# Kernel tuning notes

Measured on AMD Instinct MI355X. Metric: run time of the kernel, lower is better.

## Reference

```python
import jax, jax.numpy as jnp
import numpy as np

B, C, A, N = 4, 128, 64, 4096


def setup_inputs() -> dict:
    key = jax.random.key(0)
    ks = jax.random.split(key, 7)
    x = jax.random.normal(ks[0], (B, C, N), dtype=jnp.float32)
    # Conv1d kernel_size=1 == pointwise linear; store weights as [out, in]
    s = 1.0 / np.sqrt(C)
    Wq = jax.random.uniform(ks[1], (A, C), jnp.float32, -s, s)
    bq = jax.random.uniform(ks[2], (A,), jnp.float32, -s, s)
    Wk = jax.random.uniform(ks[3], (A, C), jnp.float32, -s, s)
    bk = jax.random.uniform(ks[4], (A,), jnp.float32, -s, s)
    Wv = jax.random.uniform(ks[5], (C, C), jnp.float32, -s, s)
    bv = jax.random.uniform(ks[6], (C,), jnp.float32, -s, s)
    return {"x": x, "Wq": Wq, "bq": bq, "Wk": Wk, "bk": bk, "Wv": Wv, "bv": bv}


def reference(x, Wq, bq, Wk, bk, Wv, bv):
    # 1x1 conv projections: [B,C,N] -> [B,A,N] / [B,C,N]
    q = jnp.einsum('ac,bcn->ban', Wq, x) + bq[None, :, None]
    k = jnp.einsum('ac,bcn->ban', Wk, x) + bk[None, :, None]
    v = jnp.einsum('oc,bcn->bon', Wv, x) + bv[None, :, None]
    # scores: q^T k -> [B, N, N], softmax over last dim (keys)
    attn = jax.nn.softmax(jnp.einsum('ban,bam->bnm', q, k), axis=-1)
    # out = attn @ v^T -> [B, N, C], transpose back to [B, C, N]
    ctx = jnp.einsum('bnm,bcm->bcn', attn, v)
    return x + ctx
```

## Files before the change

kernel.cpp:

```cpp
#include <hip/hip_runtime.h>
#include <stdint.h>

#define BB 4
#define CC 128
#define AA 64
#define NN 4096
#define LOG2E 1.44269504088896f

using half8  = __attribute__((ext_vector_type(8))) _Float16;
using f32x4  = __attribute__((ext_vector_type(4))) float;
using f32x16 = __attribute__((ext_vector_type(16))) float;
using u32x4  = __attribute__((ext_vector_type(4))) uint32_t;

__device__ __forceinline__ float fexp2(float x) {
  float r; asm("v_exp_f32 %0, %1" : "=v"(r) : "v"(x)); return r;
}


__global__ __launch_bounds__(256) void proj_kernel(
    const float* __restrict__ x,
    const float* __restrict__ Wq, const float* __restrict__ bq,
    const float* __restrict__ Wk, const float* __restrict__ bk,
    const float* __restrict__ Wv, const float* __restrict__ bv,
    _Float16* __restrict__ qfrag, _Float16* __restrict__ kfrag,
    _Float16* __restrict__ vfrag)
{
  __shared__ _Float16 xT[64][136];
  __shared__ _Float16 bounce[4][64][72];
  const int tid = threadIdx.x;
  const int wid = tid >> 6, lane = tid & 63;
  const int g = lane >> 4, lr = lane & 15;
  const int c32 = lane & 31, h = lane >> 5;
  const int b = blockIdx.x & 3, nt = blockIdx.x >> 2;
  const int n0 = nt * 64;

  for (int i = 0; i < 8; ++i) {
    int idx = i * 256 + tid;
    int c = idx >> 4, s = idx & 15;
    float4 xv = *(const float4*)(x + (size_t)(b * CC + c) * NN + n0 + s * 4);
    xT[s*4+0][c] = (_Float16)xv.x;
    xT[s*4+1][c] = (_Float16)xv.y;
    xT[s*4+2][c] = (_Float16)xv.z;
    xT[s*4+3][c] = (_Float16)xv.w;
  }
  __syncthreads();

  const float* Wp; const float* bp; int rbase;
  if (wid == 0)      { Wp = Wq; bp = bq; rbase = 0; }
  else if (wid == 1) { Wp = Wk; bp = bk; rbase = 0; }
  else               { Wp = Wv; bp = bv; rbase = (wid - 2) * 64; }
  const float oscale = (wid == 0) ? LOG2E : 1.0f;

  const f32x4 zero4 = {0.f, 0.f, 0.f, 0.f};
  f32x4 acc[4][4];
  #pragma unroll
  for (int i = 0; i < 4; ++i)
    #pragma unroll
    for (int j = 0; j < 4; ++j) acc[i][j] = zero4;

  #pragma unroll
  for (int ks = 0; ks < 4; ++ks) {
    half8 af[4];
    #pragma unroll
    for (int nf = 0; nf < 4; ++nf)
      af[nf] = *(const half8*)&xT[nf*16 + lr][ks*32 + g*8];
    half8 bfr[4];
    #pragma unroll
    for (int rf = 0; rf < 4; ++rf) {
      const float* wrow = Wp + (size_t)(rbase + rf*16 + lr) * CC + ks*32 + g*8;
      float4 w0 = *(const float4*)wrow;
      float4 w1 = *(const float4*)(wrow + 4);
      half8 t;
      t[0]=(_Float16)w0.x; t[1]=(_Float16)w0.y; t[2]=(_Float16)w0.z; t[3]=(_Float16)w0.w;
      t[4]=(_Float16)w1.x; t[5]=(_Float16)w1.y; t[6]=(_Float16)w1.z; t[7]=(_Float16)w1.w;
      bfr[rf] = t;
    }
    #pragma unroll
    for (int nf = 0; nf < 4; ++nf)
      #pragma unroll
      for (int rf = 0; rf < 4; ++rf)
        acc[nf][rf] = __builtin_amdgcn_mfma_f32_16x16x32_f16(af[nf], bfr[rf], acc[nf][rf], 0, 0, 0);
  }

  #pragma unroll
  for (int rf = 0; rf < 4; ++rf) {
    float bias = bp[rbase + rf*16 + lr];
    #pragma unroll
    for (int nf = 0; nf < 4; ++nf)
      #pragma unroll
      for (int r = 0; r < 4; ++r) {
        float val = (acc[nf][rf][r] + bias) * oscale;
        if (wid < 2) bounce[wid][nf*16 + 4*g + r][rf*16 + lr] = (_Float16)val;
        else         bounce[wid][rf*16 + lr][nf*16 + 4*g + r] = (_Float16)val;
      }
  }
  __syncthreads();

  if (wid == 0) {
    _Float16* dst = qfrag + (size_t)(b*128 + 2*nt) * 2048;
    #pragma unroll
    for (int t = 0; t < 8; ++t) {
      int n32t = t >> 2, ks = t & 3;
      half8 v8 = *(const half8*)&bounce[0][n32t*32 + c32][ks*16 + h*8];
      *(half8*)(dst + (size_t)(n32t*4 + ks)*512 + lane*8) = v8;
    }
  } else if (wid == 1) {
    _Float16* dst = kfrag + (size_t)(b*64 + nt) * 4096;
    #pragma unroll
    for (int t = 0; t < 8; ++t) {
      int mt = t >> 2, ks = t & 3;
      half8 v8 = *(const half8*)&bounce[1][mt*32 + c32][ks*16 + h*8];
      *(half8*)(dst + (size_t)(mt*4 + ks)*512 + lane*8) = v8;
    }
  } else {
    _Float16* dst = vfrag + (size_t)(b*64 + nt) * 8192;
    #pragma unroll
    for (int t = 0; t < 8; ++t) {
      int ms = t >> 1, ctl = t & 1;
      int ct = (wid - 2)*2 + ctl;
      half8 v8 = *(const half8*)&bounce[wid][ctl*32 + c32][ms*16 + h*8];
      *(half8*)(dst + (size_t)(ms*4 + ct)*512 + lane*8) = v8;
    }
  }
}

__global__ __launch_bounds__(512, 2) void attn_kernel(
    const float* __restrict__ x,
    const _Float16* __restrict__ qfrag, const _Float16* __restrict__ kfrag,
    const _Float16* __restrict__ vfrag, float* __restrict__ out)
{
  __shared__ __align__(16) float smem_f[24576 + 384 + 8448];
  float* ctxb  = smem_f;
  float* statb = smem_f + 24576;
  float* ctxw  = smem_f + 24960;

  const int tid = threadIdx.x;
  const int wid = tid >> 6, lane = tid & 63;
  const int c32 = lane & 31;
  const int h = lane >> 5;
  const bool hb = (h != 0);
  const int sub = wid >> 2;
  const int qr  = wid & 3;
  const int b = blockIdx.x & 3, qt = blockIdx.x >> 2;
  const int n0 = qt * 64;

  half8 qf[4];
  const _Float16* qfb = qfrag + (size_t)(b*128 + qt*2 + sub) * 2048;
  #pragma unroll
  for (int ks = 0; ks < 4; ++ks)
    qf[ks] = *(const half8*)(qfb + ks*512 + lane*8);

  const _Float16* kfb = kfrag + (size_t)(b*64 + qr*16) * 4096;
  const _Float16* vfb = vfrag + (size_t)(b*64 + qr*16) * 8192;

  f32x16 ctx[4];
  #pragma unroll
  for (int ct = 0; ct < 4; ++ct)
    #pragma unroll
    for (int r = 0; r < 16; ++r) ctx[ct][r] = 0.f;
  float run_m = -1e30f, run_l = 0.f;

  half8 kf[2][4];
  #pragma unroll
  for (int mt = 0; mt < 2; ++mt)
    #pragma unroll
    for (int ks = 0; ks < 4; ++ks)
      kf[mt][ks] = *(const half8*)(kfb + (size_t)(mt*4 + ks)*512 + lane*8);

  for (int it = 0; it < 16; ++it) {
    const _Float16* vt = vfb + (size_t)it * 8192;
    half8 vfA[2][4];
    #pragma unroll
    for (int ms = 0; ms < 2; ++ms)
      #pragma unroll
      for (int ct = 0; ct < 4; ++ct)
        vfA[ms][ct] = *(const half8*)(vt + (size_t)(ms*4 + ct)*512 + lane*8);

    f32x16 s[2];
    #pragma unroll
    for (int mt = 0; mt < 2; ++mt)
      #pragma unroll
      for (int r = 0; r < 16; ++r) s[mt][r] = 0.f;
    #pragma unroll
    for (int ks = 0; ks < 4; ++ks) {
      s[0] = __builtin_amdgcn_mfma_f32_32x32x16_f16(kf[0][ks], qf[ks], s[0], 0, 0, 0);
      s[1] = __builtin_amdgcn_mfma_f32_32x32x16_f16(kf[1][ks], qf[ks], s[1], 0, 0, 0);
    }

    half8 vfB[2][4];
    #pragma unroll
    for (int ms = 0; ms < 2; ++ms)
      #pragma unroll
      for (int ct = 0; ct < 4; ++ct)
        vfB[ms][ct] = *(const half8*)(vt + (size_t)((ms+2)*4 + ct)*512 + lane*8);
    {
      const _Float16* kn = kfb + (size_t)(((it + 1) & 15)) * 4096;
      #pragma unroll
      for (int mt = 0; mt < 2; ++mt)
        #pragma unroll
        for (int ks = 0; ks < 4; ++ks)
          kf[mt][ks] = *(const half8*)(kn + (size_t)(mt*4 + ks)*512 + lane*8);
    }

    float tm = s[0][0];
    #pragma unroll
    for (int r = 1; r < 16; ++r) tm = fmaxf(tm, s[0][r]);
    #pragma unroll
    for (int r = 0; r < 16; ++r) tm = fmaxf(tm, s[1][r]);
    float tmf = fmaxf(tm, __shfl_xor(tm, 32));
    if (!__all(tmf <= run_m + 8.f)) {
      float nm = fmaxf(run_m, tmf);
      float corr = fexp2(run_m - nm);
      run_m = nm;
      run_l *= corr;
      float cr[16];
      #pragma unroll
      for (int r = 0; r < 16; ++r) {
        int nr = (r & 3) + 8*(r >> 2) + 4*h;
        cr[r] = __shfl(corr, nr);
      }
      #pragma unroll
      for (int ct = 0; ct < 4; ++ct)
        #pragma unroll
        for (int r = 0; r < 16; ++r) ctx[ct][r] *= cr[r];
    }

    float rs = 0.f;
    half8 pa4[4];
    #pragma unroll
    for (int mt = 0; mt < 2; ++mt) {
      uint32_t u[8];
      #pragma unroll
      for (int i = 0; i < 8; ++i) {
        float pa_ = fexp2(s[mt][2*i]   - run_m);
        float pb_ = fexp2(s[mt][2*i+1] - run_m);
        rs += pa_ + pb_;
        u[i] = __builtin_bit_cast(uint32_t, __builtin_amdgcn_cvt_pkrtz(pa_, pb_));
      }
      uint32_t t02 = __shfl_xor(hb ? u[0] : u[2], 32);
      uint32_t t13 = __shfl_xor(hb ? u[1] : u[3], 32);
      uint32_t t46 = __shfl_xor(hb ? u[4] : u[6], 32);
      uint32_t t57 = __shfl_xor(hb ? u[5] : u[7], 32);
      u32x4 w0 = { hb ? t02 : u[0], hb ? t13 : u[1],
                   hb ? u[2] : t02, hb ? u[3] : t13 };
      u32x4 w1 = { hb ? t46 : u[4], hb ? t57 : u[5],
                   hb ? u[6] : t46, hb ? u[7] : t57 };
      pa4[2*mt]   = __builtin_bit_cast(half8, w0);
      pa4[2*mt+1] = __builtin_bit_cast(half8, w1);
    }
    rs += __shfl_xor(rs, 32);
    run_l += rs;

    #pragma unroll
    for (int ms = 0; ms < 2; ++ms)
      #pragma unroll
      for (int ct = 0; ct < 4; ++ct)
        ctx[ct] = __builtin_amdgcn_mfma_f32_32x32x16_f16(pa4[ms], vfA[ms][ct], ctx[ct], 0, 0, 0);
    #pragma unroll
    for (int ms = 0; ms < 2; ++ms)
      #pragma unroll
      for (int ct = 0; ct < 4; ++ct)
        ctx[ct] = __builtin_amdgcn_mfma_f32_32x32x16_f16(pa4[ms+2], vfB[ms][ct], ctx[ct], 0, 0, 0);
  }

  if (qr != 0) {
    const int slot = sub*3 + (qr - 1);
    #pragma unroll
    for (int ct = 0; ct < 4; ++ct)
      #pragma unroll
      for (int r = 0; r < 16; ++r)
        ctxb[slot*4096 + (ct*16 + r)*64 + lane] = ctx[ct][r];
    if (h == 0) {
      statb[slot*64 + c32*2 + 0] = run_m;
      statb[slot*64 + c32*2 + 1] = run_l;
    }
  }
  __syncthreads();

  if (qr == 0) {
    float m_w[4], l_w[4];
    m_w[0] = run_m; l_w[0] = run_l;
    #pragma unroll
    for (int w = 1; w < 4; ++w) {
      const int slot = sub*3 + (w - 1);
      m_w[w] = statb[slot*64 + c32*2 + 0];
      l_w[w] = statb[slot*64 + c32*2 + 1];
    }
    float M = fmaxf(fmaxf(m_w[0], m_w[1]), fmaxf(m_w[2], m_w[3]));
    float sc[4], L = 0.f;
    #pragma unroll
    for (int w = 0; w < 4; ++w) { sc[w] = fexp2(m_w[w] - M); L += l_w[w]*sc[w]; }
    float inv = 1.0f / L;
    float a0[16], a1[16], a2[16], a3[16], ai[16];
    #pragma unroll
    for (int r = 0; r < 16; ++r) {
      int nr = (r & 3) + 8*(r >> 2) + 4*h;
      a0[r] = __shfl(sc[0], nr); a1[r] = __shfl(sc[1], nr);
      a2[r] = __shfl(sc[2], nr); a3[r] = __shfl(sc[3], nr);
      ai[r] = __shfl(inv, nr);
    }
    #pragma unroll
    for (int ct = 0; ct < 4; ++ct)
      #pragma unroll
      for (int r = 0; r < 16; ++r) {
        int nr = (r & 3) + 8*(r >> 2) + 4*h;
        float vmrg = ctx[ct][r]*a0[r]
                   + ctxb[(sub*3 + 0)*4096 + (ct*16 + r)*64 + lane]*a1[r]
                   + ctxb[(sub*3 + 1)*4096 + (ct*16 + r)*64 + lane]*a2[r]
                   + ctxb[(sub*3 + 2)*4096 + (ct*16 + r)*64 + lane]*a3[r];
        ctxw[(sub*32 + nr)*132 + ct*32 + c32] = vmrg * ai[r];
      }
  }
  __syncthreads();

  {
    const int c  = tid >> 2;
    const int nl = (tid & 3) * 16;
    const float* xr   = x   + (size_t)(b*CC + c)*NN + n0 + nl;
    float*       orow = out + (size_t)(b*CC + c)*NN + n0 + nl;
    #pragma unroll
    for (int i4 = 0; i4 < 4; ++i4) {
      float4 xv = *(const float4*)(xr + i4*4);
      float4 o;
      o.x = xv.x + ctxw[(nl + i4*4 + 0)*132 + c];
      o.y = xv.y + ctxw[(nl + i4*4 + 1)*132 + c];
      o.z = xv.z + ctxw[(nl + i4*4 + 2)*132 + c];
      o.w = xv.w + ctxw[(nl + i4*4 + 3)*132 + c];
      *(float4*)(orow + i4*4) = o;
    }
  }
}

extern "C" void kernel_launch(void* const* d_in, const int* in_sizes, int n_in,
                              void* d_out, int out_size, void* d_ws, size_t ws_size,
                              hipStream_t stream) {
  const float* x  = (const float*)d_in[0];
  const float* Wq = (const float*)d_in[1];
  const float* bq = (const float*)d_in[2];
  const float* Wk = (const float*)d_in[3];
  const float* bk = (const float*)d_in[4];
  const float* Wv = (const float*)d_in[5];
  const float* bv = (const float*)d_in[6];
  float* out = (float*)d_out;

  _Float16* qfrag = (_Float16*)d_ws;
  _Float16* kfrag = qfrag + (size_t)BB * 128 * 2048;
  _Float16* vfrag = kfrag + (size_t)BB * 64 * 4096;

  proj_kernel<<<dim3(BB * (NN/64)), dim3(256), 0, stream>>>(
      x, Wq, bq, Wk, bk, Wv, bv, qfrag, kfrag, vfrag);
  attn_kernel<<<dim3(BB * (NN/64)), dim3(512), 0, stream>>>(
      x, qfrag, kfrag, vfrag, out);
}
```

Measured before the change: 57.97 us.

## Double-buffer V fragments across iterations and raise MFMA wave priority

```diff
diff --git a/kernel.cpp b/kernel.cpp
--- a/kernel.cpp
+++ b/kernel.cpp
@@ -167,34 +167,44 @@
     for (int ks = 0; ks < 4; ++ks)
       kf[mt][ks] = *(const half8*)(kfb + (size_t)(mt*4 + ks)*512 + lane*8);
 
-  for (int it = 0; it < 16; ++it) {
-    const _Float16* vt = vfb + (size_t)it * 8192;
-    half8 vfA[2][4];
+  half8 vA0[2][4], vB0[2][4], vA1[2][4], vB1[2][4];
+  #pragma unroll
+  for (int ms = 0; ms < 2; ++ms)
+    #pragma unroll
+    for (int ct = 0; ct < 4; ++ct) {
+      vA0[ms][ct] = *(const half8*)(vfb + (size_t)(ms*4 + ct)*512 + lane*8);
+      vB0[ms][ct] = *(const half8*)(vfb + (size_t)((ms+2)*4 + ct)*512 + lane*8);
+    }
+
+  auto body = [&](int it, half8 (&vAc)[2][4], half8 (&vBc)[2][4],
+                          half8 (&vAn)[2][4], half8 (&vBn)[2][4]) {
+    const _Float16* vtn = vfb + (size_t)((it + 1) & 15) * 8192;
     #pragma unroll
     for (int ms = 0; ms < 2; ++ms)
       #pragma unroll
       for (int ct = 0; ct < 4; ++ct)
-        vfA[ms][ct] = *(const half8*)(vt + (size_t)(ms*4 + ct)*512 + lane*8);
+        vAn[ms][ct] = *(const half8*)(vtn + (size_t)(ms*4 + ct)*512 + lane*8);
 
     f32x16 s[2];
     #pragma unroll
     for (int mt = 0; mt < 2; ++mt)
       #pragma unroll
       for (int r = 0; r < 16; ++r) s[mt][r] = 0.f;
+    __builtin_amdgcn_s_setprio(1);
     #pragma unroll
     for (int ks = 0; ks < 4; ++ks) {
       s[0] = __builtin_amdgcn_mfma_f32_32x32x16_f16(kf[0][ks], qf[ks], s[0], 0, 0, 0);
       s[1] = __builtin_amdgcn_mfma_f32_32x32x16_f16(kf[1][ks], qf[ks], s[1], 0, 0, 0);
     }
-
-    half8 vfB[2][4];
+    __builtin_amdgcn_s_setprio(0);
+
     #pragma unroll
     for (int ms = 0; ms < 2; ++ms)
       #pragma unroll
       for (int ct = 0; ct < 4; ++ct)
-        vfB[ms][ct] = *(const half8*)(vt + (size_t)((ms+2)*4 + ct)*512 + lane*8);
+        vBn[ms][ct] = *(const half8*)(vtn + (size_t)((ms+2)*4 + ct)*512 + lane*8);
     {
-      const _Float16* kn = kfb + (size_t)(((it + 1) & 15)) * 4096;
+      const _Float16* kn = kfb + (size_t)((it + 1) & 15) * 4096;
       #pragma unroll
       for (int mt = 0; mt < 2; ++mt)
         #pragma unroll
@@ -202,11 +212,15 @@
           kf[mt][ks] = *(const half8*)(kn + (size_t)(mt*4 + ks)*512 + lane*8);
     }
 
-    float tm = s[0][0];
-    #pragma unroll
-    for (int r = 1; r < 16; ++r) tm = fmaxf(tm, s[0][r]);
-    #pragma unroll
-    for (int r = 0; r < 16; ++r) tm = fmaxf(tm, s[1][r]);
+    float t8[8];
+    #pragma unroll
+    for (int r = 0; r < 8; ++r)
+      t8[r] = fmaxf(fmaxf(s[0][r], s[0][r+8]), fmaxf(s[1][r], s[1][r+8]));
+    #pragma unroll
+    for (int off = 4; off > 0; off >>= 1)
+      #pragma unroll
+      for (int r = 0; r < off; ++r) t8[r] = fmaxf(t8[r], t8[r+off]);
+    float tm = t8[0];
     float tmf = fmaxf(tm, __shfl_xor(tm, 32));
     if (!__all(tmf <= run_m + 8.f)) {
       float nm = fmaxf(run_m, tmf);
@@ -251,16 +265,24 @@
     rs += __shfl_xor(rs, 32);
     run_l += rs;
 
+    __builtin_amdgcn_s_setprio(1);
     #pragma unroll
     for (int ms = 0; ms < 2; ++ms)
       #pragma unroll
       for (int ct = 0; ct < 4; ++ct)
-        ctx[ct] = __builtin_amdgcn_mfma_f32_32x32x16_f16(pa4[ms], vfA[ms][ct], ctx[ct], 0, 0, 0);
+        ctx[ct] = __builtin_amdgcn_mfma_f32_32x32x16_f16(pa4[ms], vAc[ms][ct], ctx[ct], 0, 0, 0);
     #pragma unroll
     for (int ms = 0; ms < 2; ++ms)
       #pragma unroll
       for (int ct = 0; ct < 4; ++ct)
-        ctx[ct] = __builtin_amdgcn_mfma_f32_32x32x16_f16(pa4[ms+2], vfB[ms][ct], ctx[ct], 0, 0, 0);
+        ctx[ct] = __builtin_amdgcn_mfma_f32_32x32x16_f16(pa4[ms+2], vBc[ms][ct], ctx[ct], 0, 0, 0);
+    __builtin_amdgcn_s_setprio(0);
+  };
+
+  #pragma unroll 1
+  for (int itt = 0; itt < 16; itt += 2) {
+    body(itt,     vA0, vB0, vA1, vB1);
+    body(itt + 1, vA1, vB1, vA0, vB0);
   }
 
   if (qr != 0) {
```

New measurement: 107.4 us. 85.3% more time.

## Double-buffer V fragments across iterations and raise MFMA wave priority

Applied to the files above, without the earlier changes.

```diff
diff --git a/kernel.cpp b/kernel.cpp
--- a/kernel.cpp
+++ b/kernel.cpp
@@ -167,101 +167,125 @@
     for (int ks = 0; ks < 4; ++ks)
       kf[mt][ks] = *(const half8*)(kfb + (size_t)(mt*4 + ks)*512 + lane*8);
 
-  for (int it = 0; it < 16; ++it) {
-    const _Float16* vt = vfb + (size_t)it * 8192;
-    half8 vfA[2][4];
-    #pragma unroll
-    for (int ms = 0; ms < 2; ++ms)
-      #pragma unroll
-      for (int ct = 0; ct < 4; ++ct)
-        vfA[ms][ct] = *(const half8*)(vt + (size_t)(ms*4 + ct)*512 + lane*8);
-
-    f32x16 s[2];
-    #pragma unroll
-    for (int mt = 0; mt < 2; ++mt)
-      #pragma unroll
-      for (int r = 0; r < 16; ++r) s[mt][r] = 0.f;
-    #pragma unroll
-    for (int ks = 0; ks < 4; ++ks) {
-      s[0] = __builtin_amdgcn_mfma_f32_32x32x16_f16(kf[0][ks], qf[ks], s[0], 0, 0, 0);
-      s[1] = __builtin_amdgcn_mfma_f32_32x32x16_f16(kf[1][ks], qf[ks], s[1], 0, 0, 0);
-    }
-
-    half8 vfB[2][4];
-    #pragma unroll
-    for (int ms = 0; ms < 2; ++ms)
-      #pragma unroll
-      for (int ct = 0; ct < 4; ++ct)
-        vfB[ms][ct] = *(const half8*)(vt + (size_t)((ms+2)*4 + ct)*512 + lane*8);
-    {
-      const _Float16* kn = kfb + (size_t)(((it + 1) & 15)) * 4096;
-      #pragma unroll
-      for (int mt = 0; mt < 2; ++mt)
-        #pragma unroll
-        for (int ks = 0; ks < 4; ++ks)
-          kf[mt][ks] = *(const half8*)(kn + (size_t)(mt*4 + ks)*512 + lane*8);
-    }
-
-    float tm = s[0][0];
-    #pragma unroll
-    for (int r = 1; r < 16; ++r) tm = fmaxf(tm, s[0][r]);
-    #pragma unroll
-    for (int r = 0; r < 16; ++r) tm = fmaxf(tm, s[1][r]);
-    float tmf = fmaxf(tm, __shfl_xor(tm, 32));
-    if (!__all(tmf <= run_m + 8.f)) {
-      float nm = fmaxf(run_m, tmf);
-      float corr = fexp2(run_m - nm);
-      run_m = nm;
-      run_l *= corr;
-      float cr[16];
-      #pragma unroll
-      for (int r = 0; r < 16; ++r) {
-        int nr = (r & 3) + 8*(r >> 2) + 4*h;
-        cr[r] = __shfl(corr, nr);
-      }
-      #pragma unroll
-      for (int ct = 0; ct < 4; ++ct)
-        #pragma unroll
-        for (int r = 0; r < 16; ++r) ctx[ct][r] *= cr[r];
-    }
-
-    float rs = 0.f;
-    half8 pa4[4];
-    #pragma unroll
-    for (int mt = 0; mt < 2; ++mt) {
-      uint32_t u[8];
-      #pragma unroll
-      for (int i = 0; i < 8; ++i) {
-        float pa_ = fexp2(s[mt][2*i]   - run_m);
-        float pb_ = fexp2(s[mt][2*i+1] - run_m);
-        rs += pa_ + pb_;
-        u[i] = __builtin_bit_cast(uint32_t, __builtin_amdgcn_cvt_pkrtz(pa_, pb_));
-      }
-      uint32_t t02 = __shfl_xor(hb ? u[0] : u[2], 32);
-      uint32_t t13 = __shfl_xor(hb ? u[1] : u[3], 32);
-      uint32_t t46 = __shfl_xor(hb ? u[4] : u[6], 32);
-      uint32_t t57 = __shfl_xor(hb ? u[5] : u[7], 32);
-      u32x4 w0 = { hb ? t02 : u[0], hb ? t13 : u[1],
-                   hb ? u[2] : t02, hb ? u[3] : t13 };
-      u32x4 w1 = { hb ? t46 : u[4], hb ? t57 : u[5],
-                   hb ? u[6] : t46, hb ? u[7] : t57 };
-      pa4[2*mt]   = __builtin_bit_cast(half8, w0);
-      pa4[2*mt+1] = __builtin_bit_cast(half8, w1);
-    }
-    rs += __shfl_xor(rs, 32);
-    run_l += rs;
-
-    #pragma unroll
-    for (int ms = 0; ms < 2; ++ms)
-      #pragma unroll
-      for (int ct = 0; ct < 4; ++ct)
-        ctx[ct] = __builtin_amdgcn_mfma_f32_32x32x16_f16(pa4[ms], vfA[ms][ct], ctx[ct], 0, 0, 0);
-    #pragma unroll
-    for (int ms = 0; ms < 2; ++ms)
-      #pragma unroll
-      for (int ct = 0; ct < 4; ++ct)
-        ctx[ct] = __builtin_amdgcn_mfma_f32_32x32x16_f16(pa4[ms+2], vfB[ms][ct], ctx[ct], 0, 0, 0);
-  }
+  half8 vA0[2][4], vB0[2][4], vA1[2][4], vB1[2][4];
+  #pragma unroll
+  for (int ms = 0; ms < 2; ++ms)
+    #pragma unroll
+    for (int ct = 0; ct < 4; ++ct) {
+      vA0[ms][ct] = *(const half8*)(vfb + (size_t)(ms*4 + ct)*512 + lane*8);
+      vB0[ms][ct] = *(const half8*)(vfb + (size_t)((ms+2)*4 + ct)*512 + lane*8);
+    }
+
+#define ITER_BODY(IT, vAc, vBc, vAn, vBn)                                      \
+  {                                                                            \
+    const _Float16* vtn = vfb + (size_t)(((IT) + 1) & 15) * 8192;              \
+          \
+    _Pragma("unroll")                                                          \
+    for (int ms = 0; ms < 2; ++ms)                                             \
+      _Pragma("unroll")                                                        \
+      for (int ct = 0; ct < 4; ++ct)                                           \
+        vAn[ms][ct] = *(const half8*)(vtn + (size_t)(ms*4 + ct)*512 + lane*8); \
+      \
+    f32x16 s[2];                                                               \
+    _Pragma("unroll")                                                          \
+    for (int mt = 0; mt < 2; ++mt)                                             \
+      _Pragma("unroll")                                                        \
+      for (int r = 0; r < 16; ++r) s[mt][r] = 0.f;                             \
+    __builtin_amdgcn_s_setprio(1);                                             \
+    _Pragma("unroll")                                                          \
+    for (int ks = 0; ks < 4; ++ks) {                                           \
+      s[0] = __builtin_amdgcn_mfma_f32_32x32x16_f16(kf[0][ks], qf[ks], s[0], 0, 0, 0); \
+      s[1] = __builtin_amdgcn_mfma_f32_32x32x16_f16(kf[1][ks], qf[ks], s[1], 0, 0, 0); \
+    }                                                                          \
+    __builtin_amdgcn_s_setprio(0);                                             \
+         \
+    _Pragma("unroll")                                                          \
+    for (int ms = 0; ms < 2; ++ms)                                             \
+      _Pragma("unroll")                                                        \
+      for (int ct = 0; ct < 4; ++ct)                                           \
+        vBn[ms][ct] = *(const half8*)(vtn + (size_t)((ms+2)*4 + ct)*512 + lane*8); \
+    {                                                                          \
+      const _Float16* kn = kfb + (size_t)(((IT) + 1) & 15) * 4096;             \
+      _Pragma("unroll")                                                        \
+      for (int mt = 0; mt < 2; ++mt)                                           \
+        _Pragma("unroll")                                                      \
+        for (int ks = 0; ks < 4; ++ks)                                         \
+          kf[mt][ks] = *(const half8*)(kn + (size_t)(mt*4 + ks)*512 + lane*8); \
+    }                                                                          \
+                              \
+    float t8[8];                                                               \
+    _Pragma("unroll")                                                          \
+    for (int r = 0; r < 8; ++r)                                                \
+      t8[r] = fmaxf(fmaxf(s[0][r], s[0][r+8]), fmaxf(s[1][r], s[1][r+8]));     \
+    _Pragma("unroll")                                                          \
+    for (int off = 4; off > 0; off >>= 1)                                      \
+      _Pragma("unroll")                                                        \
+      for (int r = 0; r < off; ++r) t8[r] = fmaxf(t8[r], t8[r+off]);           \
+    float tm = t8[0];                                                          \
+    float tmf = fmaxf(tm, __shfl_xor(tm, 32));                                 \
+    if (!__all(tmf <= run_m + 8.f)) {                                          \
+      float nm = fmaxf(run_m, tmf);                                            \
+      float corr = fexp2(run_m - nm);                                          \
+      run_m = nm;                                                              \
+      run_l *= corr;                                                           \
+      float cr[16];                                                            \
+      _Pragma("unroll")                                                        \
+      for (int r = 0; r < 16; ++r) {                                           \
+        int nr = (r & 3) + 8*(r >> 2) + 4*h;                                   \
+        cr[r] = __shfl(corr, nr);                                              \
+      }                                                                        \
+      _Pragma("unroll")                                                        \
+      for (int ct = 0; ct < 4; ++ct)                                           \
+        _Pragma("unroll")                                                      \
+        for (int r = 0; r < 16; ++r) ctx[ct][r] *= cr[r];                      \
+    }                                                                          \
+           \
+    float rs = 0.f;                                                            \
+    half8 pa4[4];                                                              \
+    _Pragma("unroll")                                                          \
+    for (int mt = 0; mt < 2; ++mt) {                                           \
+      uint32_t u[8];                                                           \
+      _Pragma("unroll")                                                        \
+      for (int i = 0; i < 8; ++i) {                                            \
+        float pa_ = fexp2(s[mt][2*i]   - run_m);                               \
+        float pb_ = fexp2(s[mt][2*i+1] - run_m);                               \
+        rs += pa_ + pb_;                                                       \
+        u[i] = __builtin_bit_cast(uint32_t, __builtin_amdgcn_cvt_pkrtz(pa_, pb_)); \
+      }                                                                        \
+      uint32_t t02 = __shfl_xor(hb ? u[0] : u[2], 32);                         \
+      uint32_t t13 = __shfl_xor(hb ? u[1] : u[3], 32);                         \
+      uint32_t t46 = __shfl_xor(hb ? u[4] : u[6], 32);                         \
+      uint32_t t57 = __shfl_xor(hb ? u[5] : u[7], 32);                         \
+      u32x4 w0 = { hb ? t02 : u[0], hb ? t13 : u[1],                           \
+                   hb ? u[2] : t02, hb ? u[3] : t13 };                         \
+      u32x4 w1 = { hb ? t46 : u[4], hb ? t57 : u[5],                           \
+                   hb ? u[6] : t46, hb ? u[7] : t57 };                         \
+      pa4[2*mt]   = __builtin_bit_cast(half8, w0);                             \
+      pa4[2*mt+1] = __builtin_bit_cast(half8, w1);                             \
+    }                                                                          \
+    rs += __shfl_xor(rs, 32);                                                  \
+    run_l += rs;                                                               \
+        \
+    __builtin_amdgcn_s_setprio(1);                                             \
+    _Pragma("unroll")                                                          \
+    for (int ms = 0; ms < 2; ++ms)                                             \
+      _Pragma("unroll")                                                        \
+      for (int ct = 0; ct < 4; ++ct)                                           \
+        ctx[ct] = __builtin_amdgcn_mfma_f32_32x32x16_f16(pa4[ms], vAc[ms][ct], ctx[ct], 0, 0, 0); \
+    _Pragma("unroll")                                                          \
+    for (int ms = 0; ms < 2; ++ms)                                             \
+      _Pragma("unroll")                                                        \
+      for (int ct = 0; ct < 4; ++ct)                                           \
+        ctx[ct] = __builtin_amdgcn_mfma_f32_32x32x16_f16(pa4[ms+2], vBc[ms][ct], ctx[ct], 0, 0, 0); \
+    __builtin_amdgcn_s_setprio(0);                                             \
+  }
+
+  #pragma unroll 1
+  for (int itt = 0; itt < 16; itt += 2) {
+    ITER_BODY(itt,     vA0, vB0, vA1, vB1)
+    ITER_BODY(itt + 1, vA1, vB1, vA0, vB0)
+  }
+#undef ITER_BODY
 
   if (qr != 0) {
     const int slot = sub*3 + (qr - 1);
```

New measurement: 107.5 us. +85.5%, slower.
